# Performance work log

Hardware: AMD Instinct MI355X
Metric: run time of the kernel (lower is better)

Reference implementation:

```python
import jax, jax.numpy as jnp
import numpy as np

N = 50000        # total nodes
E = 600000       # total edges (before self loops)
NID = 16         # node_input_dim
D = 128          # hidden_dim
H = 4            # heads
C = D // H       # out_channels per head = 32
L = 4            # num_layers
EPS = 1e-5
NEG_SLOPE = 0.2


def setup_inputs() -> dict:
    key = jax.random.key(0)
    ks = jax.random.split(key, 16)
    s = 0.05
    return {
        "node_types": jax.random.randint(ks[0], (N,), 0, 3),
        "edge_index": jax.random.randint(ks[1], (2, E), 0, N),
        # embedding + input projection (Linear -> LayerNorm -> ReLU)
        "emb_table": jax.random.normal(ks[2], (3, NID), jnp.float32) * s,
        "proj_W": jax.random.normal(ks[3], (NID, D), jnp.float32) * s,
        "proj_b": jnp.zeros((D,), jnp.float32),
        "proj_g": jnp.ones((D,), jnp.float32),
        "proj_beta": jnp.zeros((D,), jnp.float32),
        # per-layer GATv2 params (stacked over L layers)
        "Wl": jax.random.normal(ks[4], (L, D, D), jnp.float32) * s,   # lin_l weight
        "bl": jnp.zeros((L, D), jnp.float32),                          # lin_l bias
        "Wr": jax.random.normal(ks[5], (L, D, D), jnp.float32) * s,   # lin_r weight
        "br": jnp.zeros((L, D), jnp.float32),                          # lin_r bias
        "att": jax.random.normal(ks[6], (L, H, C), jnp.float32) * s,  # attention vector
        "gat_bias": jnp.zeros((L, D), jnp.float32),                   # output bias (concat)
        # per-layer LayerNorm
        "ln_g": jnp.ones((L, D), jnp.float32),
        "ln_b": jnp.zeros((L, D), jnp.float32),
    }


def layer_norm(x, g, b):
    mu = jnp.mean(x, axis=-1, keepdims=True)
    var = jnp.mean(jnp.square(x - mu), axis=-1, keepdims=True)
    return (x - mu) * jax.lax.rsqrt(var + EPS) * g + b


def gatv2_layer(x, src, dst, Wl, bl, Wr, br, att, bias):
    # x: [N, D]; src/dst: [E+N] (self loops included)
    n = x.shape[0]
    xl = (x @ Wl + bl).reshape(n, H, C)   # source transform
    xr = (x @ Wr + br).reshape(n, H, C)   # destination transform
    e = jax.nn.leaky_relu(xl[src] + xr[dst], NEG_SLOPE)          # [E', H, C]
    logits = jnp.einsum('ehc,hc->eh', e, att)                    # [E', H]
    m = jax.ops.segment_max(logits, dst, num_segments=n)         # segment softmax (stable)
    alpha = jnp.exp(logits - m[dst])
    denom = jax.ops.segment_sum(alpha, dst, num_segments=n)
    alpha = alpha / denom[dst]                                   # [E', H]
    msg = xl[src] * alpha[:, :, None]                            # [E', H, C]
    out = jax.ops.segment_sum(msg, dst, num_segments=n)          # [N, H, C]
    return out.reshape(n, H * C) + bias


def reference(node_types, edge_index, emb_table, proj_W, proj_b, proj_g, proj_beta,
              Wl, bl, Wr, br, att, gat_bias, ln_g, ln_b):
    n = node_types.shape[0]
    loop = jnp.arange(n, dtype=edge_index.dtype)
    src = jnp.concatenate([edge_index[0], loop])   # add self loops
    dst = jnp.concatenate([edge_index[1], loop])

    x = emb_table[node_types]                      # [N, NID]
    x = jax.nn.relu(layer_norm(x @ proj_W + proj_b, proj_g, proj_beta))  # input_proj (dropout=id at eval)

    for i in range(L):
        x_res = x
        x = gatv2_layer(x, src, dst, Wl[i], bl[i], Wr[i], br[i], att[i], gat_bias[i])
        x = layer_norm(x + x_res, ln_g[i], ln_b[i])
        x = jax.nn.relu(x)
    return x
```

## Files before the change

kernel.cpp:

```cpp
#include <hip/hip_runtime.h>
#include <hip/hip_bf16.h>
#include <math.h>

#define D      128
#define NID    16
#define H      4
#define CH     32
#define NLAYER 4
#define EPS    1e-5f
#define NEG    0.2f
#define LOG2E  1.442695040888963f

typedef __attribute__((ext_vector_type(8))) short short8;
typedef __attribute__((ext_vector_type(4))) float floatx4;
typedef _Float16 h2 __attribute__((ext_vector_type(2)));
typedef float fx2 __attribute__((ext_vector_type(2)));

__device__ __forceinline__ float2 bf2_to_f2(unsigned int u) {
    float2 r;
    unsigned int lo = u << 16;
    unsigned int hi = u & 0xffff0000u;
    r.x = __uint_as_float(lo);
    r.y = __uint_as_float(hi);
    return r;
}

__device__ __forceinline__ unsigned short f2bf(float f) {
    __hip_bfloat16 h = __float2bfloat16(f);
    return *reinterpret_cast<unsigned short*>(&h);
}

__device__ __forceinline__ unsigned short f2h(float f) {
    _Float16 h = (_Float16)f;
    unsigned short u;
    __builtin_memcpy(&u, &h, 2);
    return u;
}

__device__ __forceinline__ h2 u2h2(unsigned int u) {
    h2 v;
    __builtin_memcpy(&v, &u, 4);
    return v;
}

__device__ __forceinline__ h2 pkrtz(float a, float b) {
    auto r = __builtin_amdgcn_cvt_pkrtz(a, b);
    h2 out;
    __builtin_memcpy(&out, &r, 4);
    return out;
}

__device__ __forceinline__ unsigned char f2fp8(float v) {
    int pk = __builtin_amdgcn_cvt_pk_fp8_f32(v, v, 0, false);
    return (unsigned char)(pk & 0xff);
}

__device__ __forceinline__ void fp8x4_to_h2x2(unsigned int w, h2* out) {
    fx2 f0 = __builtin_amdgcn_cvt_pk_f32_fp8((int)w, false);
    fx2 f1 = __builtin_amdgcn_cvt_pk_f32_fp8((int)w, true);
    out[0] = pkrtz(f0[0], f0[1]);
    out[1] = pkrtz(f1[0], f1[1]);
}


__global__ __launch_bounds__(256) void scan_blocks_kernel(const int* __restrict__ deg, int* __restrict__ offs,
                                                          int* __restrict__ bsum, int n) {
    __shared__ int sw[8];
    int t = threadIdx.x;
    int i = blockIdx.x * 256 + t;
    int v = (i < n) ? deg[i] + 1 : 0;
    int lane = t & 63, w = t >> 6;
    int x = v;
    #pragma unroll
    for (int off = 1; off < 64; off <<= 1) {
        int y = __shfl_up(x, off, 64);
        if (lane >= off) x += y;
    }
    if (lane == 63) sw[w] = x;
    __syncthreads();
    if (t == 0) {
        int s = 0;
        for (int k = 0; k < 4; ++k) { int tv = sw[k]; sw[k] = s; s += tv; }
        sw[4] = s;
    }
    __syncthreads();
    int excl = x - v + sw[w];
    if (i < n) offs[i] = excl;
    if (t == 255) bsum[blockIdx.x] = sw[4];
}

__global__ __launch_bounds__(256) void scan_add_kernel(int* __restrict__ offs, const int* __restrict__ bsum,
                                                       int* __restrict__ cursor, int n, int nb, int total) {
    __shared__ int sw[8];
    __shared__ int sS;
    int t = threadIdx.x;
    int bid = blockIdx.x;
    int v = (t < bid && t < nb) ? bsum[t] : 0;
    int lane = t & 63, w = t >> 6;
    #pragma unroll
    for (int off = 32; off > 0; off >>= 1) v += __shfl_xor(v, off, 64);
    if (lane == 0) sw[w] = v;
    __syncthreads();
    if (t == 0) sS = sw[0] + sw[1] + sw[2] + sw[3];
    __syncthreads();
    int S = sS;
    int i = bid * 256 + t;
    if (i < n) {
        int o = offs[i] + S;
        offs[i] = o;
        cursor[i] = o;
    }
    if (i == 0) offs[n] = total;
}

__global__ __launch_bounds__(256) void setup_kernel(
    const int* __restrict__ types, const float* __restrict__ emb,
    const float* __restrict__ W, const float* __restrict__ b,
    const float* __restrict__ g, const float* __restrict__ beta,
    unsigned short* __restrict__ x,
    const float* __restrict__ Wl, const float* __restrict__ Wr,
    unsigned short* __restrict__ wt,
    const int* __restrict__ dsts, int* __restrict__ deg, int e,
    int n, int nbEmbed) {
    __shared__ float sW[NID * D];
    __shared__ float semb[3 * NID];
    int blk = blockIdx.x;
    int t = threadIdx.x;
    if (blk < nbEmbed) {
        for (int i = t; i < NID * D; i += 256) sW[i] = W[i];
        for (int i = t; i < 3 * NID; i += 256) semb[i] = emb[i];
        __syncthreads();
        int lane = t & 63, w = t >> 6;
        int node = blk * 4 + w;
        if (node >= n) return;
        int c0 = 2 * lane;
        int ty = types[node];
        const float* ev = &semb[ty * NID];
        float v0 = b[c0], v1 = b[c0 + 1];
        #pragma unroll
        for (int k = 0; k < NID; ++k) {
            float ek = ev[k];
            v0 = fmaf(ek, sW[k * D + c0], v0);
            v1 = fmaf(ek, sW[k * D + c0 + 1], v1);
        }
        float s = v0 + v1, sq = v0 * v0 + v1 * v1;
        #pragma unroll
        for (int off = 1; off < 64; off <<= 1) {
            s  += __shfl_xor(s, off, 64);
            sq += __shfl_xor(sq, off, 64);
        }
        float mu  = s * (1.0f / D);
        float var = sq * (1.0f / D) - mu * mu;
        float r   = rsqrtf(var + EPS);
        v0 = fmaxf((v0 - mu) * r * g[c0]     + beta[c0],     0.0f);
        v1 = fmaxf((v1 - mu) * r * g[c0 + 1] + beta[c0 + 1], 0.0f);
        unsigned int packed = (unsigned int)f2bf(v0) | ((unsigned int)f2bf(v1) << 16);
        *(unsigned int*)(x + (size_t)node * D + c0) = packed;
    } else if (blk < nbEmbed + 512) {
        int idx = (blk - nbEmbed) * 256 + t;
        int k    = idx & (D - 1);
        int nrow = (idx >> 7) & (D - 1);
        int s    = (idx >> 14) & 1;
        int l    = idx >> 15;
        const float* Wm = s ? Wr : Wl;
        wt[idx] = f2bf(Wm[(size_t)l * D * D + (size_t)k * D + nrow]);
    } else {
        int i = (blk - nbEmbed - 512) * 256 + t;
        if (i < e) atomicAdd(&deg[dsts[i]], 1);
    }
}

__global__ __launch_bounds__(256) void dual_gemm_mfma_kernel(
    const unsigned short* __restrict__ x, const unsigned short* __restrict__ wt,
    const float* __restrict__ bl, const float* __restrict__ br,
    unsigned char* __restrict__ xl, unsigned short* __restrict__ xr, int n,
    int ntiles,
    const int* __restrict__ srcs, const int* __restrict__ dsts, int e,
    int* __restrict__ cursor, int* __restrict__ csr_src) {
    __shared__ __align__(16) unsigned short sa[64 * 136];
    int t = threadIdx.x;
    if (blockIdx.x >= ntiles) {
        int i = (blockIdx.x - ntiles) * 256 + t;
        if (i < e) {
            int pos = atomicAdd(&cursor[dsts[i]], 1);
            csr_src[pos] = srcs[i];
        } else if (i < e + n) {
            int node = i - e;
            int pos = atomicAdd(&cursor[node], 1);
            csr_src[pos] = node;
        }
        return;
    }
    int nbase = blockIdx.x * 64;
    int rows = n - nbase; if (rows > 64) rows = 64;
    int lane = t & 63, w = t >> 6;
    int L = lane & 15, q = lane >> 4;
    int s  = w >> 1;
    int n0 = (w & 1) * 64;
    const unsigned short* wb = wt + ((size_t)s * D + n0) * D;
    short8 b[4][4];
    #pragma unroll
    for (int kk = 0; kk < 4; ++kk)
        #pragma unroll
        for (int ni = 0; ni < 4; ++ni)
            b[kk][ni] = *(const short8*)(wb + (size_t)(ni * 16 + L) * D + kk * 32 + q * 8);
    {
        int r   = t >> 2;
        int seg = t & 3;
        uint4* drow = (uint4*)(sa + r * 136 + seg * 32);
        if (r < rows) {
            const uint4* srow = (const uint4*)(x + (size_t)(nbase + r) * D + seg * 32);
            drow[0] = srow[0]; drow[1] = srow[1]; drow[2] = srow[2]; drow[3] = srow[3];
        } else {
            uint4 z = make_uint4(0, 0, 0, 0);
            drow[0] = z; drow[1] = z; drow[2] = z; drow[3] = z;
        }
    }
    __syncthreads();
    floatx4 acc[4][4];
    #pragma unroll
    for (int mi = 0; mi < 4; ++mi)
        #pragma unroll
        for (int ni = 0; ni < 4; ++ni)
            acc[mi][ni] = (floatx4){0.0f, 0.0f, 0.0f, 0.0f};
    #pragma unroll
    for (int kk = 0; kk < 4; ++kk) {
        int ko = kk * 32 + q * 8;
        short8 a[4];
        #pragma unroll
        for (int mi = 0; mi < 4; ++mi)
            a[mi] = *(const short8*)(sa + (mi * 16 + L) * 136 + ko);
        #pragma unroll
        for (int mi = 0; mi < 4; ++mi)
            #pragma unroll
            for (int ni = 0; ni < 4; ++ni)
                acc[mi][ni] = __builtin_amdgcn_mfma_f32_16x16x32_bf16(a[mi], b[kk][ni], acc[mi][ni], 0, 0, 0);
    }
    const float* bias = s ? br : bl;
    __syncthreads();
    if (s == 0) {
        unsigned char* sb = (unsigned char*)sa;
        #pragma unroll
        for (int ni = 0; ni < 4; ++ni) {
            int col = n0 + ni * 16 + L;
            float bv = bias[col];
            #pragma unroll
            for (int mi = 0; mi < 4; ++mi) {
                #pragma unroll
                for (int r = 0; r < 4; ++r) {
                    int row = mi * 16 + q * 4 + r;
                    sb[row * 272 + col] = f2fp8(acc[mi][ni][r] + bv);
                }
            }
        }
    }
    __syncthreads();
    {
        unsigned char* sb = (unsigned char*)sa;
        #pragma unroll
        for (int c = 0; c < 2; ++c) {
            int chunk = c * 256 + t;
            int row   = chunk >> 3;
            int off   = (chunk & 7) * 16;
            if (row < rows) {
                uint4 v = *(const uint4*)(sb + row * 272 + off);
                *(uint4*)(xl + (size_t)(nbase + row) * D + off) = v;
            }
        }
    }
    __syncthreads();
    if (s == 1) {
        #pragma unroll
        for (int ni = 0; ni < 4; ++ni) {
            int col = n0 + ni * 16 + L;
            float bv = bias[col];
            #pragma unroll
            for (int mi = 0; mi < 4; ++mi) {
                #pragma unroll
                for (int r = 0; r < 4; ++r) {
                    int row = mi * 16 + q * 4 + r;
                    sa[row * 136 + col] = f2h(acc[mi][ni][r] + bv);
                }
            }
        }
    }
    __syncthreads();
    #pragma unroll
    for (int c = 0; c < 4; ++c) {
        int chunk = c * 256 + t;
        int row   = chunk >> 4;
        int off   = (chunk & 15) * 8;
        if (row < rows) {
            short8 v = *(const short8*)(sa + row * 136 + off);
            *(short8*)(xr + (size_t)(nbase + row) * D + off) = v;
        }
    }
}

__global__ __launch_bounds__(256) void gat_agg_kernel(
    const unsigned char* __restrict__ xl, const unsigned short* __restrict__ xr,
    const unsigned short* __restrict__ xin,
    const int* __restrict__ offs, const int* __restrict__ csr_src,
    const float* __restrict__ att,
    const float* __restrict__ gbias,
    const float* __restrict__ lng, const float* __restrict__ lnb,
    unsigned short* __restrict__ xout_bf, float* __restrict__ xout_f32, int n) {
    int t = threadIdx.x;
    int lane = t & 63, w = t >> 6;
    int node = blockIdx.x * 4 + w;
    if (node >= n) return;
    int g  = lane >> 4;
    int l  = lane & 15;
    int cb = l * 8;
    h2 xr2[4], at2[4];
    {
        uint4 u = *(const uint4*)(xr + (size_t)node * D + cb);
        xr2[0] = u2h2(u.x); xr2[1] = u2h2(u.y); xr2[2] = u2h2(u.z); xr2[3] = u2h2(u.w);
        float4 t0 = *(const float4*)(att + cb);
        float4 t1 = *(const float4*)(att + cb + 4);
        at2[0] = (h2){(_Float16)(t0.x * LOG2E), (_Float16)(t0.y * LOG2E)};
        at2[1] = (h2){(_Float16)(t0.z * LOG2E), (_Float16)(t0.w * LOG2E)};
        at2[2] = (h2){(_Float16)(t1.x * LOG2E), (_Float16)(t1.y * LOG2E)};
        at2[3] = (h2){(_Float16)(t1.z * LOG2E), (_Float16)(t1.w * LOG2E)};
    }
    h2 acch[4];
    #pragma unroll
    for (int i = 0; i < 4; ++i) acch[i] = (h2){(_Float16)0.0f, (_Float16)0.0f};
    float lsum = 0.0f;
    int s0 = offs[node], s1 = offs[node + 1];
    int j0 = s0 + g;
    bool val_c = j0 < s1;
    int src_c = csr_src[val_c ? j0 : s0];
    uint2 u_c = *(const uint2*)(xl + (size_t)src_c * D + cb);
    int j1 = j0 + 4;
    bool val_n = j1 < s1;
    int src_n = csr_src[val_n ? j1 : s0];
    uint2 u_n = *(const uint2*)(xl + (size_t)src_n * D + cb);
    int j2 = j0 + 8;
    bool val_2 = j2 < s1;
    int src_2 = csr_src[val_2 ? j2 : s0];
    for (int j = s0; j < s1; j += 4) {
        uint2 u_2 = *(const uint2*)(xl + (size_t)src_2 * D + cb);
        int j3 = j + 12 + g;
        bool val_3 = j3 < s1;
        int src_3 = csr_src[val_3 ? j3 : s0];
        h2 xv2[4];
        fp8x4_to_h2x2(u_c.x, xv2);
        fp8x4_to_h2x2(u_c.y, xv2 + 2);
        float p = 0.0f;
        #pragma unroll
        for (int i = 0; i < 4; ++i) {
            h2 e  = xv2[i] + xr2[i];
            h2 el = __builtin_elementwise_max(e, e * (_Float16)NEG);
            p = __builtin_amdgcn_fdot2(el, at2[i], p, false);
        }
        p += __shfl_xor(p, 1, 64);
        p += __shfl_xor(p, 2, 64);
        float wgt = val_c ? exp2f(p) : 0.0f;
        lsum += wgt;
        _Float16 wh = (_Float16)wgt;
        h2 w2 = {wh, wh};
        #pragma unroll
        for (int i = 0; i < 4; ++i) acch[i] += w2 * xv2[i];
        u_c = u_n; u_n = u_2;
        val_c = val_n; val_n = val_2;
        val_2 = val_3; src_2 = src_3;
    }
    float acc[8];
    #pragma unroll
    for (int i = 0; i < 4; ++i) {
        acc[2 * i]     = (float)acch[i][0];
        acc[2 * i + 1] = (float)acch[i][1];
    }
    #pragma unroll
    for (int i = 0; i < 8; ++i) {
        acc[i] += __shfl_xor(acc[i], 16, 64);
        acc[i] += __shfl_xor(acc[i], 32, 64);
    }
    lsum += __shfl_xor(lsum, 16, 64);
    lsum += __shfl_xor(lsum, 32, 64);
    float inv = 1.0f / lsum;
    float xi[8];
    {
        uint4 u = *(const uint4*)(xin + (size_t)node * D + cb);
        float2 a = bf2_to_f2(u.x), b = bf2_to_f2(u.y), c = bf2_to_f2(u.z), d = bf2_to_f2(u.w);
        xi[0]=a.x; xi[1]=a.y; xi[2]=b.x; xi[3]=b.y; xi[4]=c.x; xi[5]=c.y; xi[6]=d.x; xi[7]=d.y;
    }
    float4 gb0 = *(const float4*)(gbias + cb);
    float4 gb1 = *(const float4*)(gbias + cb + 4);
    float gb[8] = {gb0.x, gb0.y, gb0.z, gb0.w, gb1.x, gb1.y, gb1.z, gb1.w};
    float v[8];
    #pragma unroll
    for (int i = 0; i < 8; ++i) v[i] = fmaf(acc[i], inv, gb[i] + xi[i]);
    float s = 0.0f, sq = 0.0f;
    #pragma unroll
    for (int i = 0; i < 8; ++i) { s += v[i]; sq = fmaf(v[i], v[i], sq); }
    #pragma unroll
    for (int off = 1; off < 16; off <<= 1) {
        s  += __shfl_xor(s, off, 64);
        sq += __shfl_xor(sq, off, 64);
    }
    float mu  = s * (1.0f / D);
    float var = sq * (1.0f / D) - mu * mu;
    float r   = rsqrtf(var + EPS);
    float4 lg0 = *(const float4*)(lng + cb);
    float4 lg1 = *(const float4*)(lng + cb + 4);
    float4 lb0 = *(const float4*)(lnb + cb);
    float4 lb1 = *(const float4*)(lnb + cb + 4);
    float lg[8] = {lg0.x, lg0.y, lg0.z, lg0.w, lg1.x, lg1.y, lg1.z, lg1.w};
    float lb[8] = {lb0.x, lb0.y, lb0.z, lb0.w, lb1.x, lb1.y, lb1.z, lb1.w};
    float o[8];
    #pragma unroll
    for (int i = 0; i < 8; ++i) o[i] = fmaxf((v[i] - mu) * r * lg[i] + lb[i], 0.0f);
    if (g == 0) {
        if (xout_f32) {
            *(float4*)(xout_f32 + (size_t)node * D + cb)     = make_float4(o[0], o[1], o[2], o[3]);
            *(float4*)(xout_f32 + (size_t)node * D + cb + 4) = make_float4(o[4], o[5], o[6], o[7]);
        } else {
            unsigned int p0 = (unsigned int)f2bf(o[0]) | ((unsigned int)f2bf(o[1]) << 16);
            unsigned int p1 = (unsigned int)f2bf(o[2]) | ((unsigned int)f2bf(o[3]) << 16);
            unsigned int p2 = (unsigned int)f2bf(o[4]) | ((unsigned int)f2bf(o[5]) << 16);
            unsigned int p3 = (unsigned int)f2bf(o[6]) | ((unsigned int)f2bf(o[7]) << 16);
            *(uint4*)(xout_bf + (size_t)node * D + cb) = make_uint4(p0, p1, p2, p3);
        }
    }
}

extern "C" void kernel_launch(void* const* d_in, const int* in_sizes, int n_in,
                              void* d_out, int out_size, void* d_ws, size_t ws_size,
                              hipStream_t stream) {
    const int*   node_types = (const int*)d_in[0];
    const int*   edge_index = (const int*)d_in[1];
    const float* emb        = (const float*)d_in[2];
    const float* projW      = (const float*)d_in[3];
    const float* projb      = (const float*)d_in[4];
    const float* projg      = (const float*)d_in[5];
    const float* projbeta   = (const float*)d_in[6];
    const float* Wl         = (const float*)d_in[7];
    const float* bl         = (const float*)d_in[8];
    const float* Wr         = (const float*)d_in[9];
    const float* br         = (const float*)d_in[10];
    const float* att        = (const float*)d_in[11];
    const float* gbias      = (const float*)d_in[12];
    const float* lng        = (const float*)d_in[13];
    const float* lnb        = (const float*)d_in[14];
    float* out = (float*)d_out;

    int n = in_sizes[0];
    int e = in_sizes[1] / 2;
    const int* srcs = edge_index;
    const int* dsts = edge_index + e;

    char* p = (char*)d_ws;
    auto carve = [&](size_t bytes) {
        char* q = p;
        p += (bytes + 255) & ~(size_t)255;
        return q;
    };
    int*   deg     = (int*)carve((size_t)n * 4);
    int*   offs    = (int*)carve((size_t)(n + 1) * 4);
    int*   cursor  = (int*)carve((size_t)n * 4);
    int*   bsum    = (int*)carve(256 * 4);
    int*   csr_src = (int*)carve((size_t)(e + n) * 4);
    unsigned short* xbuf = (unsigned short*)carve((size_t)n * D * 2);
    unsigned char*  xlb  = (unsigned char*)carve((size_t)n * D);
    unsigned short* xrb  = (unsigned short*)carve((size_t)n * D * 2);
    unsigned short* wt   = (unsigned short*)carve((size_t)NLAYER * 2 * D * D * 2);

    int nb = (n + 255) / 256;
    int nbEmbed = (n + 3) / 4;
    int nbE = (e + 255) / 256;
    int ntiles = (n + 63) / 64;
    int nscat  = (e + n + 255) / 256;

    hipMemsetAsync(deg, 0, (size_t)n * 4, stream);

    setup_kernel<<<nbEmbed + 512 + nbE, 256, 0, stream>>>(
        node_types, emb, projW, projb, projg, projbeta, xbuf,
        Wl, Wr, wt, dsts, deg, e, n, nbEmbed);

    scan_blocks_kernel<<<nb, 256, 0, stream>>>(deg, offs, bsum, n);
    scan_add_kernel<<<nb, 256, 0, stream>>>(offs, bsum, cursor, n, nb, e + n);

    for (int layer = 0; layer < NLAYER; ++layer) {
        int extra = (layer == 0) ? nscat : 0;
        dual_gemm_mfma_kernel<<<ntiles + extra, 256, 0, stream>>>(
            xbuf, wt + (size_t)layer * 2 * D * D,
            bl + (size_t)layer * D, br + (size_t)layer * D, xlb, xrb, n,
            ntiles, srcs, dsts, e, cursor, csr_src);
        bool last = (layer == NLAYER - 1);
        gat_agg_kernel<<<(n + 3) / 4, 256, 0, stream>>>(
            xlb, xrb, xbuf, offs, csr_src,
            att + (size_t)layer * H * CH, gbias + (size_t)layer * D,
            lng + (size_t)layer * D, lnb + (size_t)layer * D,
            last ? (unsigned short*)nullptr : xbuf, last ? out : (float*)nullptr, n);
    }
}
```

Baseline: 393.7 us.

## Exploit three node types: precompute layer-0 projections per type, skip first GEMM

Before layer 0, a node's features depend only on its type, which takes one of three values. So the input projection and the layer-0 lin_l/lin_r transforms are computed for just three rows in a single setup block. The layer-0 aggregation reads those rows by type, which is packed into the top bits of each CSR source entry, and the first dual GEMM and the per-node embedding pass are dropped. The scatter moves out of the GEMM launch into its own kernel. The cost is extra bit-masking of CSR entries in every layer, and correctness depends on node indices fitting in 28 bits.

```diff
diff --git a/kernel.cpp b/kernel.cpp
--- a/kernel.cpp
+++ b/kernel.cpp
@@ -10,6 +10,7 @@
 #define EPS    1e-5f
 #define NEG    0.2f
 #define LOG2E  1.442695040888963f
+#define SRCMASK 0x0FFFFFFF
 
 typedef __attribute__((ext_vector_type(8))) short short8;
 typedef __attribute__((ext_vector_type(4))) float floatx4;
@@ -113,84 +114,115 @@
     if (i == 0) offs[n] = total;
 }
 
+__global__ __launch_bounds__(256) void scatter_kernel(
+    const int* __restrict__ srcs, const int* __restrict__ dsts,
+    const int* __restrict__ types,
+    int e, int n, int* cursor, int* __restrict__ csr_src) {
+    int i = blockIdx.x * blockDim.x + threadIdx.x;
+    if (i < e) {
+        int s = srcs[i];
+        int ty = types[s];
+        int pos = atomicAdd(&cursor[dsts[i]], 1);
+        csr_src[pos] = s | (ty << 28);
+    } else if (i < e + n) {
+        int node = i - e;
+        int ty = types[node];
+        int pos = atomicAdd(&cursor[node], 1);
+        csr_src[pos] = node | (ty << 28);
+    }
+}
+
 __global__ __launch_bounds__(256) void setup_kernel(
-    const int* __restrict__ types, const float* __restrict__ emb,
-    const float* __restrict__ W, const float* __restrict__ b,
-    const float* __restrict__ g, const float* __restrict__ beta,
-    unsigned short* __restrict__ x,
+    const float* __restrict__ emb,
+    const float* __restrict__ W, const float* __restrict__ pb,
+    const float* __restrict__ pg, const float* __restrict__ pbeta,
     const float* __restrict__ Wl, const float* __restrict__ Wr,
+    const float* __restrict__ bl, const float* __restrict__ br,
     unsigned short* __restrict__ wt,
     const int* __restrict__ dsts, int* __restrict__ deg, int e,
-    int n, int nbEmbed) {
-    __shared__ float sW[NID * D];
+    unsigned short* __restrict__ x3bf, unsigned char* __restrict__ xl3,
+    unsigned short* __restrict__ xr3,
+    int nbE) {
+    __shared__ float sbuf[NID * D];
     __shared__ float semb[3 * NID];
     int blk = blockIdx.x;
     int t = threadIdx.x;
-    if (blk < nbEmbed) {
-        for (int i = t; i < NID * D; i += 256) sW[i] = W[i];
-        for (int i = t; i < 3 * NID; i += 256) semb[i] = emb[i];
-        __syncthreads();
-        int lane = t & 63, w = t >> 6;
-        int node = blk * 4 + w;
-        if (node >= n) return;
-        int c0 = 2 * lane;
-        int ty = types[node];
-        const float* ev = &semb[ty * NID];
-        float v0 = b[c0], v1 = b[c0 + 1];
-        #pragma unroll
-        for (int k = 0; k < NID; ++k) {
-            float ek = ev[k];
-            v0 = fmaf(ek, sW[k * D + c0], v0);
-            v1 = fmaf(ek, sW[k * D + c0 + 1], v1);
-        }
-        float s = v0 + v1, sq = v0 * v0 + v1 * v1;
-        #pragma unroll
-        for (int off = 1; off < 64; off <<= 1) {
-            s  += __shfl_xor(s, off, 64);
-            sq += __shfl_xor(sq, off, 64);
-        }
-        float mu  = s * (1.0f / D);
-        float var = sq * (1.0f / D) - mu * mu;
-        float r   = rsqrtf(var + EPS);
-        v0 = fmaxf((v0 - mu) * r * g[c0]     + beta[c0],     0.0f);
-        v1 = fmaxf((v1 - mu) * r * g[c0 + 1] + beta[c0 + 1], 0.0f);
-        unsigned int packed = (unsigned int)f2bf(v0) | ((unsigned int)f2bf(v1) << 16);
-        *(unsigned int*)(x + (size_t)node * D + c0) = packed;
-    } else if (blk < nbEmbed + 512) {
-        int idx = (blk - nbEmbed) * 256 + t;
+    if (blk < 512) {
+        int idx = blk * 256 + t;
         int k    = idx & (D - 1);
         int nrow = (idx >> 7) & (D - 1);
         int s    = (idx >> 14) & 1;
         int l    = idx >> 15;
         const float* Wm = s ? Wr : Wl;
         wt[idx] = f2bf(Wm[(size_t)l * D * D + (size_t)k * D + nrow]);
+    } else if (blk < 512 + nbE) {
+        int i = (blk - 512) * 256 + t;
+        if (i < e) atomicAdd(&deg[dsts[i]], 1);
     } else {
-        int i = (blk - nbEmbed - 512) * 256 + t;
-        if (i < e) atomicAdd(&deg[dsts[i]], 1);
+        float* p3  = sbuf;
+        float* x3s = sbuf + 384;
+        float* red = sbuf + 768;
+        for (int i = t; i < 3 * NID; i += 256) semb[i] = emb[i];
+        __syncthreads();
+        int c = t;
+        if (c < D) {
+            float wcol[NID];
+            #pragma unroll
+            for (int k = 0; k < NID; ++k) wcol[k] = W[k * D + c];
+            float bc = pb[c];
+            #pragma unroll
+            for (int ty = 0; ty < 3; ++ty) {
+                float a = bc;
+                #pragma unroll
+                for (int k = 0; k < NID; ++k) a = fmaf(semb[ty * NID + k], wcol[k], a);
+                p3[ty * D + c] = a;
+            }
+        }
+        __syncthreads();
+        #pragma unroll 1
+        for (int ty = 0; ty < 3; ++ty) {
+            float v = (c < D) ? p3[ty * D + c] : 0.0f;
+            float s = v, sq = v * v;
+            #pragma unroll
+            for (int off = 1; off < 64; off <<= 1) {
+                s  += __shfl_xor(s, off, 64);
+                sq += __shfl_xor(sq, off, 64);
+            }
+            if ((t & 63) == 0 && t < 128) { red[(t >> 6) * 2] = s; red[(t >> 6) * 2 + 1] = sq; }
+            __syncthreads();
+            float S = red[0] + red[2], SQ = red[1] + red[3];
+            float mu = S * (1.0f / D), var = SQ * (1.0f / D) - mu * mu;
+            float r = rsqrtf(var + EPS);
+            if (c < D) {
+                float o = fmaxf((p3[ty * D + c] - mu) * r * pg[c] + pbeta[c], 0.0f);
+                unsigned short bfv = f2bf(o);
+                x3s[ty * D + c] = __uint_as_float((unsigned int)bfv << 16);
+                x3bf[ty * D + c] = bfv;
+            }
+            __syncthreads();
+        }
+        if (c < D) {
+            #pragma unroll 1
+            for (int ty = 0; ty < 3; ++ty) {
+                float al = bl[c], ar = br[c];
+                for (int k = 0; k < D; ++k) {
+                    float xv = x3s[ty * D + k];
+                    al = fmaf(xv, Wl[(size_t)k * D + c], al);
+                    ar = fmaf(xv, Wr[(size_t)k * D + c], ar);
+                }
+                xl3[ty * D + c] = f2fp8(al);
+                xr3[ty * D + c] = f2h(ar);
+            }
+        }
     }
 }
 
 __global__ __launch_bounds__(256) void dual_gemm_mfma_kernel(
     const unsigned short* __restrict__ x, const unsigned short* __restrict__ wt,
     const float* __restrict__ bl, const float* __restrict__ br,
-    unsigned char* __restrict__ xl, unsigned short* __restrict__ xr, int n,
-    int ntiles,
-    const int* __restrict__ srcs, const int* __restrict__ dsts, int e,
-    int* __restrict__ cursor, int* __restrict__ csr_src) {
+    unsigned char* __restrict__ xl, unsigned short* __restrict__ xr, int n) {
     __shared__ __align__(16) unsigned short sa[64 * 136];
     int t = threadIdx.x;
-    if (blockIdx.x >= ntiles) {
-        int i = (blockIdx.x - ntiles) * 256 + t;
-        if (i < e) {
-            int pos = atomicAdd(&cursor[dsts[i]], 1);
-            csr_src[pos] = srcs[i];
-        } else if (i < e + n) {
-            int node = i - e;
-            int pos = atomicAdd(&cursor[node], 1);
-            csr_src[pos] = node;
-        }
-        return;
-    }
     int nbase = blockIdx.x * 64;
     int rows = n - nbase; if (rows > 64) rows = 64;
     int lane = t & 63, w = t >> 6;
@@ -297,9 +329,12 @@
     }
 }
 
+template<bool L0>
 __global__ __launch_bounds__(256) void gat_agg_kernel(
     const unsigned char* __restrict__ xl, const unsigned short* __restrict__ xr,
     const unsigned short* __restrict__ xin,
+    const unsigned char* __restrict__ xl3, const unsigned short* __restrict__ xr3,
+    const unsigned short* __restrict__ x3bf, const int* __restrict__ types,
     const int* __restrict__ offs, const int* __restrict__ csr_src,
     const float* __restrict__ att,
     const float* __restrict__ gbias,
@@ -312,9 +347,11 @@
     int g  = lane >> 4;
     int l  = lane & 15;
     int cb = l * 8;
+    int tyn = L0 ? types[node] : 0;
+    const unsigned short* xrrow = L0 ? (xr3 + (size_t)tyn * D) : (xr + (size_t)node * D);
     h2 xr2[4], at2[4];
     {
-        uint4 u = *(const uint4*)(xr + (size_t)node * D + cb);
+        uint4 u = *(const uint4*)(xrrow + cb);
         xr2[0] = u2h2(u.x); xr2[1] = u2h2(u.y); xr2[2] = u2h2(u.z); xr2[3] = u2h2(u.w);
         float4 t0 = *(const float4*)(att + cb);
         float4 t1 = *(const float4*)(att + cb + 4);
@@ -323,6 +360,10 @@
         at2[2] = (h2){(_Float16)(t1.x * LOG2E), (_Float16)(t1.y * LOG2E)};
         at2[3] = (h2){(_Float16)(t1.z * LOG2E), (_Float16)(t1.w * LOG2E)};
     }
+    auto rowp = [&](int v) -> const unsigned char* {
+        if (L0) return xl3 + (size_t)((v >> 28) & 3) * D;
+        return xl + (size_t)(v & SRCMASK) * D;
+    };
     h2 acch[4];
     #pragma unroll
     for (int i = 0; i < 4; ++i) acch[i] = (h2){(_Float16)0.0f, (_Float16)0.0f};
@@ -331,16 +372,16 @@
     int j0 = s0 + g;
     bool val_c = j0 < s1;
     int src_c = csr_src[val_c ? j0 : s0];
-    uint2 u_c = *(const uint2*)(xl + (size_t)src_c * D + cb);
+    uint2 u_c = *(const uint2*)(rowp(src_c) + cb);
     int j1 = j0 + 4;
     bool val_n = j1 < s1;
     int src_n = csr_src[val_n ? j1 : s0];
-    uint2 u_n = *(const uint2*)(xl + (size_t)src_n * D + cb);
+    uint2 u_n = *(const uint2*)(rowp(src_n) + cb);
     int j2 = j0 + 8;
     bool val_2 = j2 < s1;
     int src_2 = csr_src[val_2 ? j2 : s0];
     for (int j = s0; j < s1; j += 4) {
-        uint2 u_2 = *(const uint2*)(xl + (size_t)src_2 * D + cb);
+        uint2 u_2 = *(const uint2*)(rowp(src_2) + cb);
         int j3 = j + 12 + g;
         bool val_3 = j3 < s1;
         int src_3 = csr_src[val_3 ? j3 : s0];
@@ -380,9 +421,10 @@
     lsum += __shfl_xor(lsum, 16, 64);
     lsum += __shfl_xor(lsum, 32, 64);
     float inv = 1.0f / lsum;
+    const unsigned short* xinrow = L0 ? (x3bf + (size_t)tyn * D) : (xin + (size_t)node * D);
     float xi[8];
     {
-        uint4 u = *(const uint4*)(xin + (size_t)node * D + cb);
+        uint4 u = *(const uint4*)(xinrow + cb);
         float2 a = bf2_to_f2(u.x), b = bf2_to_f2(u.y), c = bf2_to_f2(u.z), d = bf2_to_f2(u.w);
         xi[0]=a.x; xi[1]=a.y; xi[2]=b.x; xi[3]=b.y; xi[4]=c.x; xi[5]=c.y; xi[6]=d.x; xi[7]=d.y;
     }
@@ -466,31 +508,37 @@
     unsigned char*  xlb  = (unsigned char*)carve((size_t)n * D);
     unsigned short* xrb  = (unsigned short*)carve((size_t)n * D * 2);
     unsigned short* wt   = (unsigned short*)carve((size_t)NLAYER * 2 * D * D * 2);
+    unsigned short* x3bf = (unsigned short*)carve(3 * D * 2);
+    unsigned char*  xl3  = (unsigned char*)carve(3 * D);
+    unsigned short* xr3  = (unsigned short*)carve(3 * D * 2);
 
     int nb = (n + 255) / 256;
-    int nbEmbed = (n + 3) / 4;
     int nbE = (e + 255) / 256;
     int ntiles = (n + 63) / 64;
     int nscat  = (e + n + 255) / 256;
 
     hipMemsetAsync(deg, 0, (size_t)n * 4, stream);
 
-    setup_kernel<<<nbEmbed + 512 + nbE, 256, 0, stream>>>(
-        node_types, emb, projW, projb, projg, projbeta, xbuf,
-        Wl, Wr, wt, dsts, deg, e, n, nbEmbed);
+    setup_kernel<<<512 + nbE + 1, 256, 0, stream>>>(
+        emb, projW, projb, projg, projbeta,
+        Wl, Wr, bl, br, wt, dsts, deg, e,
+        x3bf, xl3, xr3, nbE);
 
     scan_blocks_kernel<<<nb, 256, 0, stream>>>(deg, offs, bsum, n);
     scan_add_kernel<<<nb, 256, 0, stream>>>(offs, bsum, cursor, n, nb, e + n);
-
-    for (int layer = 0; layer < NLAYER; ++layer) {
-        int extra = (layer == 0) ? nscat : 0;
-        dual_gemm_mfma_kernel<<<ntiles + extra, 256, 0, stream>>>(
+    scatter_kernel<<<nscat, 256, 0, stream>>>(srcs, dsts, node_types, e, n, cursor, csr_src);
+
+    gat_agg_kernel<true><<<(n + 3) / 4, 256, 0, stream>>>(
+        xlb, xrb, xbuf, xl3, xr3, x3bf, node_types, offs, csr_src,
+        att, gbias, lng, lnb, xbuf, nullptr, n);
+
+    for (int layer = 1; layer < NLAYER; ++layer) {
+        dual_gemm_mfma_kernel<<<ntiles, 256, 0, stream>>>(
             xbuf, wt + (size_t)layer * 2 * D * D,
-            bl + (size_t)layer * D, br + (size_t)layer * D, xlb, xrb, n,
-            ntiles, srcs, dsts, e, cursor, csr_src);
+            bl + (size_t)layer * D, br + (size_t)layer * D, xlb, xrb, n);
         bool last = (layer == NLAYER - 1);
-        gat_agg_kernel<<<(n + 3) / 4, 256, 0, stream>>>(
-            xlb, xrb, xbuf, offs, csr_src,
+        gat_agg_kernel<false><<<(n + 3) / 4, 256, 0, stream>>>(
+            xlb, xrb, xbuf, xl3, xr3, x3bf, node_types, offs, csr_src,
             att + (size_t)layer * H * CH, gbias + (size_t)layer * D,
             lng + (size_t)layer * D, lnb + (size_t)layer * D,
             last ? (unsigned short*)nullptr : xbuf, last ? out : (float*)nullptr, n);
```

Measured after the change: 353.2 us. 1.11x faster.
